# Optimization experiments

Measured on AMD Instinct MI355X. Metric: run time of the kernel, lower is better.

## Reference

```python
import jax, jax.numpy as jnp
import numpy as np

B, S, F = 128, 256, 40
H, D, NH, L, FF = 64, 128, 4, 2, 2048
REG, BIN, NW = 8, 1, 3
NEG = -1e9


def _ln(x, s, b, eps=1e-5):
    m = x.mean(-1, keepdims=True)
    v = ((x - m) ** 2).mean(-1, keepdims=True)
    return (x - m) / jnp.sqrt(v + eps) * s + b


def setup_inputs() -> dict:
    key = jax.random.key(0)
    ks = list(jax.random.split(key, 40))
    k = iter(ks)
    def rn(shape, s=0.05):
        return jax.random.normal(next(k), shape, jnp.float32) * s
    inp = {}
    inp['x'] = jax.random.normal(next(k), (B, S, F), jnp.float32)
    inp['mask'] = jnp.ones((B, S, F), jnp.float32)
    inp['delta'] = jax.random.uniform(next(k), (B, S, F), jnp.float32)
    # GRU params (torch layout: [3H, in], gates order r,z,n)
    inp['gru_w_ih'] = rn((3 * H, 3 * F))
    inp['gru_w_hh'] = rn((3 * H, H))
    inp['gru_b_ih'] = rn((3 * H,))
    inp['gru_b_hh'] = rn((3 * H,))
    inp['dm_w'] = rn((D, H)); inp['dm_b'] = rn((D,))
    # transformer layers stacked on leading dim L
    inp['in_proj_w'] = rn((L, 3 * D, D)); inp['in_proj_b'] = rn((L, 3 * D))
    inp['out_proj_w'] = rn((L, D, D)); inp['out_proj_b'] = rn((L, D))
    inp['lin1_w'] = rn((L, FF, D)); inp['lin1_b'] = rn((L, FF))
    inp['lin2_w'] = rn((L, D, FF)); inp['lin2_b'] = rn((L, D))
    inp['ln1_s'] = jnp.ones((L, D), jnp.float32); inp['ln1_b'] = jnp.zeros((L, D), jnp.float32)
    inp['ln2_s'] = jnp.ones((L, D), jnp.float32); inp['ln2_b'] = jnp.zeros((L, D), jnp.float32)
    inp['score_w'] = rn((1, D)); inp['score_b'] = rn((1,))
    inp['reg_w'] = rn((NW, REG, D)); inp['reg_b'] = rn((NW, REG))
    inp['bin_w'] = rn((NW, BIN, D)); inp['bin_b'] = rn((NW, BIN))
    inp['window_id'] = jax.random.randint(next(k), (B,), 0, NW, jnp.int32)
    return inp


def reference(x, mask, delta, gru_w_ih, gru_w_hh, gru_b_ih, gru_b_hh, dm_w, dm_b,
              in_proj_w, in_proj_b, out_proj_w, out_proj_b, lin1_w, lin1_b,
              lin2_w, lin2_b, ln1_s, ln1_b, ln2_s, ln2_b, score_w, score_b,
              reg_w, reg_b, bin_w, bin_b, window_id):
    inp = jnp.concatenate([x, mask, delta], -1)          # [B,S,3F]
    xw = inp @ gru_w_ih.T + gru_b_ih                      # [B,S,3H] precomputed input gates

    def step(h, xw_t):
        gh = h @ gru_w_hh.T + gru_b_hh
        xr, xz, xn = jnp.split(xw_t, 3, -1)
        hr, hz, hn = jnp.split(gh, 3, -1)
        r = jax.nn.sigmoid(xr + hr)
        zg = jax.nn.sigmoid(xz + hz)
        n = jnp.tanh(xn + r * hn)
        h_new = (1.0 - zg) * n + zg * h
        return h_new, h_new

    h0 = jnp.zeros((x.shape[0], H), x.dtype)
    _, hs = jax.lax.scan(step, h0, jnp.swapaxes(xw, 0, 1))  # [S,B,H]
    z = jnp.swapaxes(hs, 0, 1) @ dm_w.T + dm_b              # [B,S,D]

    time_mask = mask.sum(-1) > 0                            # [B,S] bool
    bias = jnp.where(time_mask[:, None, None, :], 0.0, NEG).astype(z.dtype)
    dh = D // NH
    scale = 1.0 / np.sqrt(dh)

    for l in range(L):  # post-LN torch TransformerEncoderLayer
        qkv = z @ in_proj_w[l].T + in_proj_b[l]
        q, k, v = jnp.split(qkv, 3, -1)
        q = q.reshape(B, S, NH, dh).transpose(0, 2, 1, 3)
        k = k.reshape(B, S, NH, dh).transpose(0, 2, 1, 3)
        v = v.reshape(B, S, NH, dh).transpose(0, 2, 1, 3)
        attn = jax.nn.softmax(jnp.einsum('bhqd,bhkd->bhqk', q, k) * scale + bias, -1)
        o = jnp.einsum('bhqk,bhkd->bhqd', attn, v).transpose(0, 2, 1, 3).reshape(B, S, D)
        z = _ln(z + (o @ out_proj_w[l].T + out_proj_b[l]), ln1_s[l], ln1_b[l])
        ff = jax.nn.relu(z @ lin1_w[l].T + lin1_b[l]) @ lin2_w[l].T + lin2_b[l]
        z = _ln(z + ff, ln2_s[l], ln2_b[l])

    scores = (z @ score_w.T + score_b)[..., 0]              # [B,S]
    scores = jnp.where(time_mask, scores, NEG)
    alpha = jax.nn.softmax(scores, 1)
    pooled = jnp.einsum('bsd,bs->bd', z, alpha)             # [B,D]

    # routed heads: gather 1-of-3 head weights per sample, batched matvec
    y_reg = jnp.einsum('bod,bd->bo', reg_w[window_id], pooled) + reg_b[window_id]
    y_bin = jnp.einsum('bod,bd->bo', bin_w[window_id], pooled) + bin_b[window_id]
    return (y_reg, y_bin)
```

## Files before the change

### kernel.cpp

```cpp
#include <hip/hip_runtime.h>

typedef __attribute__((ext_vector_type(8))) short short8;
typedef __attribute__((ext_vector_type(4))) float f32x4;
typedef unsigned short u16;

#define BB   128
#define SS   256
#define FIN  40
#define HH   64
#define DD   128
#define NHH  4
#define LL   2
#define NEGV (-1e9f)

__device__ __forceinline__ u16 f2b(float f) {
    unsigned u = __float_as_uint(f);
    return (u16)((u + 0x7FFFu + ((u >> 16) & 1u)) >> 16);
}
__device__ __forceinline__ float b2f(u16 u) {
    return __uint_as_float(((unsigned)u) << 16);
}

__global__ __launch_bounds__(256) void cvt_all_kernel(const float* __restrict__ dm_w,
                                                      const float* __restrict__ ip_w,
                                                      const float* __restrict__ op_w,
                                                      const float* __restrict__ l1_w,
                                                      const float* __restrict__ l2_w,
                                                      u16* __restrict__ o_dm, u16* __restrict__ o_ip,
                                                      u16* __restrict__ o_op, u16* __restrict__ o_l1,
                                                      u16* __restrict__ o_l2) {
    int blk = blockIdx.x;
    const float* s; u16* d; int off;
    if      (blk < 4)   { s = dm_w; d = o_dm; off = blk; }
    else if (blk < 52)  { s = ip_w; d = o_ip; off = blk - 4; }
    else if (blk < 68)  { s = op_w; d = o_op; off = blk - 52; }
    else if (blk < 324) { s = l1_w; d = o_l1; off = blk - 68; }
    else                { s = l2_w; d = o_l2; off = blk - 324; }
    int i = (off * 256 + threadIdx.x) * 8;
    float4 a = *(const float4*)&s[i];
    float4 b = *(const float4*)&s[i + 4];
    short8 o;
    o[0] = (short)f2b(a.x); o[1] = (short)f2b(a.y); o[2] = (short)f2b(a.z); o[3] = (short)f2b(a.w);
    o[4] = (short)f2b(b.x); o[5] = (short)f2b(b.y); o[6] = (short)f2b(b.z); o[7] = (short)f2b(b.w);
    *(short8*)&d[i] = o;
}

__global__ __launch_bounds__(256) void tm_kernel(const float* __restrict__ mask,
                                                 float* __restrict__ tm) {
    int i = blockIdx.x * blockDim.x + threadIdx.x;
    if (i >= BB * SS) return;
    const float* m = mask + (size_t)i * FIN;
    float s = 0.f;
    for (int f = 0; f < FIN; ++f) s += m[f];
    tm[i] = (s > 0.f) ? 1.f : 0.f;
}

__global__ __launch_bounds__(192) void xw_kernel(const float* __restrict__ x,
                                                 const float* __restrict__ mask,
                                                 const float* __restrict__ delta,
                                                 const float* __restrict__ w_ih,
                                                 const float* __restrict__ b_ih,
                                                 float* __restrict__ xwt) {
    __shared__ float inp[16][120];
    __shared__ float wl[192][21];
    int group = blockIdx.x >> 8;
    int t = blockIdx.x & 255;
    int tid = threadIdx.x;

    for (int idx = tid; idx < 16 * 120; idx += 192) {
        int r = idx / 120, k = idx % 120;
        size_t g = (size_t)(group * 16 + r) * 256 + t;
        float v;
        if (k < 40)      v = x[g * FIN + k];
        else if (k < 80) v = mask[g * FIN + (k - 40)];
        else             v = delta[g * FIN + (k - 80)];
        inp[r][k] = v;
    }

    float acc[16];
#pragma unroll
    for (int r = 0; r < 16; ++r) acc[r] = 0.f;

    for (int kt = 0; kt < 6; ++kt) {
        __syncthreads();
        for (int idx = tid; idx < 192 * 20; idx += 192) {
            int r = idx / 20, k = idx % 20;
            wl[r][k] = w_ih[(size_t)r * 120 + kt * 20 + k];
        }
        __syncthreads();
#pragma unroll
        for (int kk = 0; kk < 20; ++kk) {
            float w = wl[tid][kk];
            int kg = kt * 20 + kk;
#pragma unroll
            for (int r = 0; r < 16; ++r) acc[r] += w * inp[r][kg];
        }
    }
    float bias = b_ih[tid];
    float* o = xwt + ((size_t)(group * 256 + t) * 192 + tid) * 16;
#pragma unroll
    for (int r = 0; r < 16; r += 4) {
        float4 v = {acc[r] + bias, acc[r + 1] + bias, acc[r + 2] + bias, acc[r + 3] + bias};
        *(float4*)&o[r] = v;
    }
}

__device__ __forceinline__ float gru_gate(float xr, float xz, float xn,
                                          float ar, float az, float an, float hold) {
    float r  = 1.f / (1.f + __expf(-(xr + ar)));
    float zg = 1.f / (1.f + __expf(-(xz + az)));
    float nx = xn + r * an;
    float n  = 2.f / (1.f + __expf(-2.f * nx)) - 1.f;
    return (1.f - zg) * n + zg * hold;
}

__global__ __launch_bounds__(512, 1) void gru_scan_kernel(const float* __restrict__ w_hh,
                                                          const float* __restrict__ b_hh,
                                                          const float* __restrict__ xwt,
                                                          u16* __restrict__ hsb) {
    __shared__ __align__(16) u16 hb[2][16 * 64];
    int b0 = blockIdx.x * 16;
    int tid = threadIdx.x;
    int w = tid >> 6, lane = tid & 63;
    int fr = lane & 15, hi = lane >> 4;
    int cw = w & 3;
    int jg = w >> 2;

    for (int idx = tid; idx < 1024; idx += 512) hb[0][idx] = 0;

    int c = cw * 16 + fr;
    float br_ = b_hh[c], bz_ = b_hh[64 + c], bn_ = b_hh[128 + c];

    short8 wfr[2], wfz[2], wfn[2];
#pragma unroll
    for (int ks = 0; ks < 2; ++ks) {
        int slot = ks * 4 + hi;
        const float* p0 = w_hh + (size_t)c * 64 + slot * 8;
        const float* p1 = w_hh + (size_t)(64 + c) * 64 + slot * 8;
        const float* p2 = w_hh + (size_t)(128 + c) * 64 + slot * 8;
#pragma unroll
        for (int q = 0; q < 8; ++q) {
            wfr[ks][q] = (short)f2b(p0[q]);
            wfz[ks][q] = (short)f2b(p1[q]);
            wfn[ks][q] = (short)f2b(p2[q]);
        }
    }

    const float* xg = xwt + (size_t)blockIdx.x * (256 * 192 * 16);
    int lo = hi * 4 + jg * 2;

    float hrA = 0.f, hrB = 0.f;

    int woA = (lo + 0) * 64 + ((((c >> 3) ^ ((lo + 0) & 7))) << 3) + (c & 7);
    int woB = (lo + 1) * 64 + ((((c >> 3) ^ ((lo + 1) & 7))) << 3) + (c & 7);
    size_t hoA = ((size_t)(b0 + lo + 0) * SS) * 64 + c;
    size_t hoB = ((size_t)(b0 + lo + 1) * SS) * 64 + c;

    float2 axr = *(const float2*)&xg[((size_t)0 * 192 + c) * 16 + lo];
    float2 axz = *(const float2*)&xg[((size_t)0 * 192 + 64 + c) * 16 + lo];
    float2 axn = *(const float2*)&xg[((size_t)0 * 192 + 128 + c) * 16 + lo];
    float2 bxr = *(const float2*)&xg[((size_t)1 * 192 + c) * 16 + lo];
    float2 bxz = *(const float2*)&xg[((size_t)1 * 192 + 64 + c) * 16 + lo];
    float2 bxn = *(const float2*)&xg[((size_t)1 * 192 + 128 + c) * 16 + lo];
    __syncthreads();

    int cur = 0;
    auto step = [&](float2 xr2, float2 xz2, float2 xn2, int t) {
        f32x4 ar = {br_, br_, br_, br_};
        f32x4 az = {bz_, bz_, bz_, bz_};
        f32x4 an = {bn_, bn_, bn_, bn_};
#pragma unroll
        for (int ks = 0; ks < 2; ++ks) {
            int soff = (((ks << 2) + hi) ^ (fr & 7)) << 3;
            short8 af = *(const short8*)&hb[cur][fr * 64 + soff];
            ar = __builtin_amdgcn_mfma_f32_16x16x32_bf16(af, wfr[ks], ar, 0, 0, 0);
            az = __builtin_amdgcn_mfma_f32_16x16x32_bf16(af, wfz[ks], az, 0, 0, 0);
            an = __builtin_amdgcn_mfma_f32_16x16x32_bf16(af, wfn[ks], an, 0, 0, 0);
        }
        float aR0, aR1, aZ0, aZ1, aN0, aN1;
        if (jg == 0) { aR0 = ar[0]; aR1 = ar[1]; aZ0 = az[0]; aZ1 = az[1]; aN0 = an[0]; aN1 = an[1]; }
        else         { aR0 = ar[2]; aR1 = ar[3]; aZ0 = az[2]; aZ1 = az[3]; aN0 = an[2]; aN1 = an[3]; }
        hrA = gru_gate(xr2.x, xz2.x, xn2.x, aR0, aZ0, aN0, hrA);
        hrB = gru_gate(xr2.y, xz2.y, xn2.y, aR1, aZ1, aN1, hrB);
        u16 v0 = f2b(hrA), v1 = f2b(hrB);
        int nxt = cur ^ 1;
        hb[nxt][woA] = v0; hb[nxt][woB] = v1;
        hsb[hoA + (size_t)t * 64] = v0;
        hsb[hoB + (size_t)t * 64] = v1;
        asm volatile("s_waitcnt lgkmcnt(0)\n\ts_barrier" ::: "memory");
        cur = nxt;
    };

    for (int t = 0; t < SS; t += 2) {
        {
            int tp = (t + 2 < SS) ? t + 2 : t;
            float2 nr = *(const float2*)&xg[((size_t)tp * 192 + c) * 16 + lo];
            float2 nz = *(const float2*)&xg[((size_t)tp * 192 + 64 + c) * 16 + lo];
            float2 nn = *(const float2*)&xg[((size_t)tp * 192 + 128 + c) * 16 + lo];
            step(axr, axz, axn, t);
            axr = nr; axz = nz; axn = nn;
        }
        {
            int tp = (t + 3 < SS) ? t + 3 : t + 1;
            float2 nr = *(const float2*)&xg[((size_t)tp * 192 + c) * 16 + lo];
            float2 nz = *(const float2*)&xg[((size_t)tp * 192 + 64 + c) * 16 + lo];
            float2 nn = *(const float2*)&xg[((size_t)tp * 192 + 128 + c) * 16 + lo];
            step(bxr, bxz, bxn, t + 1);
            bxr = nr; bxz = nz; bxn = nn;
        }
    }
}

__device__ __forceinline__ void gl_lds16(const void* g, void* s) {
    __builtin_amdgcn_global_load_lds(
        (const __attribute__((address_space(1))) void*)g,
        (__attribute__((address_space(3))) void*)s, 16, 0, 0);
}

template <int MODE, bool RELU>
__global__ __launch_bounds__(256, 2) void mfma_gemm(const u16* __restrict__ A,
                                                    const u16* __restrict__ W,
                                                    const float* __restrict__ bias,
                                                    float* __restrict__ C,
                                                    u16* __restrict__ Cb,
                                                    const float* __restrict__ lns,
                                                    const float* __restrict__ lnb,
                                                    int M, int N, int K) {
    __shared__ __align__(16) u16 Al[128 * 64];
    __shared__ __align__(16) u16 Bl[128 * 64];
    __shared__ float lred[2][2][128];
    int bm = blockIdx.x, bn = blockIdx.y;
    int tid = threadIdx.x;
    int w = tid >> 6, lane = tid & 63;
    int wrow = (w >> 1) * 64, wcol = (w & 1) * 64;
    int fr = lane & 15, hi = lane >> 4;
    int rl = lane >> 3;
    int sl = lane & 7;
    int ssl = sl ^ rl;

    const u16* Ag = A + ((size_t)bm * 128) * K + ssl * 8;
    const u16* Wg = W + ((size_t)bn * 128) * K + ssl * 8;

    f32x4 acc[4][4];
#pragma unroll
    for (int i = 0; i < 4; ++i)
#pragma unroll
        for (int jj = 0; jj < 4; ++jj) acc[i][jj] = (f32x4){0.f, 0.f, 0.f, 0.f};

    int ar[4], br[4];
#pragma unroll
    for (int m = 0; m < 4; ++m) {
        ar[m] = (wrow + m * 16 + fr) * 64;
        br[m] = (wcol + m * 16 + fr) * 64;
    }
    int swz = (fr & 7);

    for (int kt = 0; kt < K; kt += 64) {
        __syncthreads();
#pragma unroll
        for (int i = 0; i < 4; ++i) {
            int c = w * 4 + i;
            int row = c * 8 + rl;
            gl_lds16(Ag + (size_t)row * K + kt, &Al[c * 512]);
            gl_lds16(Wg + (size_t)row * K + kt, &Bl[c * 512]);
        }
        __syncthreads();
#pragma unroll
        for (int kk = 0; kk < 2; ++kk) {
            short8 a[4], bq[4];
            int soff = (((kk << 2) + hi) ^ swz) << 3;
#pragma unroll
            for (int m = 0; m < 4; ++m)
                a[m] = *(const short8*)&Al[ar[m] + soff];
#pragma unroll
            for (int n = 0; n < 4; ++n)
                bq[n] = *(const short8*)&Bl[br[n] + soff];
#pragma unroll
            for (int m = 0; m < 4; ++m)
#pragma unroll
                for (int n = 0; n < 4; ++n)
                    acc[m][n] = __builtin_amdgcn_mfma_f32_16x16x32_bf16(a[m], bq[n], acc[m][n], 0, 0, 0);
        }
    }

    float bv[4];
#pragma unroll
    for (int n = 0; n < 4; ++n) bv[n] = bias[bn * 128 + wcol + n * 16 + fr];

    if (MODE == 4) {
        float v[4][4][4];
#pragma unroll
        for (int m = 0; m < 4; ++m)
#pragma unroll
            for (int j = 0; j < 4; ++j) {
                int row = bm * 128 + wrow + m * 16 + hi * 4 + j;
#pragma unroll
                for (int n = 0; n < 4; ++n)
                    v[m][n][j] = acc[m][n][j] + bv[n] + C[(size_t)row * 128 + wcol + n * 16 + fr];
            }
#pragma unroll
        for (int m = 0; m < 4; ++m)
#pragma unroll
            for (int j = 0; j < 4; ++j) {
                float s = v[m][0][j] + v[m][1][j] + v[m][2][j] + v[m][3][j];
                float q = v[m][0][j]*v[m][0][j] + v[m][1][j]*v[m][1][j]
                        + v[m][2][j]*v[m][2][j] + v[m][3][j]*v[m][3][j];
#pragma unroll
                for (int off = 1; off <= 8; off <<= 1) {
                    s += __shfl_xor(s, off);
                    q += __shfl_xor(q, off);
                }
                if (fr == 0) {
                    int lrow = wrow + m * 16 + hi * 4 + j;
                    lred[0][w & 1][lrow] = s;
                    lred[1][w & 1][lrow] = q;
                }
            }
        __syncthreads();
        float sv[4], bb[4];
#pragma unroll
        for (int n = 0; n < 4; ++n) {
            sv[n] = lns[wcol + n * 16 + fr];
            bb[n] = lnb[wcol + n * 16 + fr];
        }
#pragma unroll
        for (int m = 0; m < 4; ++m)
#pragma unroll
            for (int j = 0; j < 4; ++j) {
                int lrow = wrow + m * 16 + hi * 4 + j;
                float mean = (lred[0][0][lrow] + lred[0][1][lrow]) * (1.f / 128.f);
                float msq  = (lred[1][0][lrow] + lred[1][1][lrow]) * (1.f / 128.f);
                float rstd = rsqrtf(msq - mean * mean + 1e-5f);
                int row = bm * 128 + lrow;
#pragma unroll
                for (int n = 0; n < 4; ++n) {
                    int col = wcol + n * 16 + fr;
                    float o = (v[m][n][j] - mean) * rstd * sv[n] + bb[n];
                    C[(size_t)row * 128 + col] = o;
                    Cb[(size_t)row * 128 + col] = f2b(o);
                }
            }
    } else {
#pragma unroll
        for (int m = 0; m < 4; ++m) {
#pragma unroll
            for (int j = 0; j < 4; ++j) {
                int row = bm * 128 + wrow + m * 16 + hi * 4 + j;
#pragma unroll
                for (int n = 0; n < 4; ++n) {
                    int col = bn * 128 + wcol + n * 16 + fr;
                    float vv = acc[m][n][j] + bv[n];
                    if (RELU) vv = fmaxf(vv, 0.f);
                    if (MODE & 1) C[(size_t)row * N + col] = vv;
                    if (MODE & 2) Cb[(size_t)row * N + col] = f2b(vv);
                }
            }
        }
    }
}

__global__ __launch_bounds__(256, 1) void ff_fused_kernel(const u16* __restrict__ zbin,
                                                          const u16* __restrict__ w1,
                                                          const float* __restrict__ b1,
                                                          const u16* __restrict__ w2,
                                                          const float* __restrict__ b2,
                                                          const float* __restrict__ lns,
                                                          const float* __restrict__ lnb,
                                                          float* __restrict__ z,
                                                          u16* __restrict__ zbout) {
    __shared__ __align__(16) u16 ZB[2][128 * 64];
    __shared__ __align__(16) u16 W1C[2][128 * 64];
    __shared__ __align__(16) u16 W2C[2][128 * 64];
    __shared__ __align__(16) u16 A1[2][128 * 64];
    __shared__ float lred[2][2][128];
    int bm = blockIdx.x;
    int tid = threadIdx.x;
    int w = tid >> 6, lane = tid & 63;
    int wrow = (w >> 1) * 64, wcol = (w & 1) * 64;
    int fr = lane & 15, hi = lane >> 4;
    int rl = lane >> 3, ssl = (lane & 7) ^ rl;
    int swz = fr & 7;
    int xh = wrow >> 6;

#pragma unroll
    for (int hk = 0; hk < 2; ++hk)
#pragma unroll
        for (int i = 0; i < 4; ++i) {
            int ch = w * 4 + i, row = ch * 8 + rl;
            gl_lds16(zbin + ((size_t)(bm * 128 + row)) * 128 + hk * 64 + ssl * 8, &ZB[hk][ch * 512]);
        }

    f32x4 acc2[4][4];
#pragma unroll
    for (int m = 0; m < 4; ++m)
#pragma unroll
        for (int n = 0; n < 4; ++n) acc2[m][n] = (f32x4){0.f, 0.f, 0.f, 0.f};

    for (int ci = 0; ci < 16; ++ci) {
#pragma unroll
        for (int hk = 0; hk < 2; ++hk)
#pragma unroll
            for (int i = 0; i < 4; ++i) {
                int ch = w * 4 + i, row = ch * 8 + rl;
                gl_lds16(w1 + ((size_t)(ci * 128 + row)) * 128 + hk * 64 + ssl * 8, &W1C[hk][ch * 512]);
                gl_lds16(w2 + ((size_t)row) * 2048 + ci * 128 + hk * 64 + ssl * 8, &W2C[hk][ch * 512]);
            }
        __syncthreads();

        f32x4 acc1[4][4];
#pragma unroll
        for (int m = 0; m < 4; ++m)
#pragma unroll
            for (int n = 0; n < 4; ++n) acc1[m][n] = (f32x4){0.f, 0.f, 0.f, 0.f};
#pragma unroll
        for (int ks = 0; ks < 4; ++ks) {
            int hk = ks >> 1;
            int soff = ((((ks & 1) << 2) + hi) ^ swz) << 3;
            short8 a[4], b[4];
#pragma unroll
            for (int m = 0; m < 4; ++m)
                a[m] = *(const short8*)&W1C[hk][(wrow + m * 16 + fr) * 64 + soff];
#pragma unroll
            for (int n = 0; n < 4; ++n)
                b[n] = *(const short8*)&ZB[hk][(wcol + n * 16 + fr) * 64 + soff];
#pragma unroll
            for (int m = 0; m < 4; ++m)
#pragma unroll
                for (int n = 0; n < 4; ++n)
                    acc1[m][n] = __builtin_amdgcn_mfma_f32_16x16x32_bf16(a[m], b[n], acc1[m][n], 0, 0, 0);
        }
#pragma unroll
        for (int m = 0; m < 4; ++m) {
            int x0 = wrow + m * 16 + hi * 4;
            float4 bb = *(const float4*)&b1[ci * 128 + x0];
            int slot = (x0 & 63) >> 3;
            int wadd = x0 & 7;
#pragma unroll
            for (int n = 0; n < 4; ++n) {
                int r = wcol + n * 16 + fr;
                float v0 = fmaxf(acc1[m][n][0] + bb.x, 0.f);
                float v1 = fmaxf(acc1[m][n][1] + bb.y, 0.f);
                float v2 = fmaxf(acc1[m][n][2] + bb.z, 0.f);
                float v3 = fmaxf(acc1[m][n][3] + bb.w, 0.f);
                uint2 pk;
                pk.x = (unsigned)f2b(v0) | ((unsigned)f2b(v1) << 16);
                pk.y = (unsigned)f2b(v2) | ((unsigned)f2b(v3) << 16);
                *(uint2*)&A1[xh][r * 64 + ((slot ^ (r & 7)) << 3) + wadd] = pk;
            }
        }
        __syncthreads();

#pragma unroll
        for (int ks = 0; ks < 4; ++ks) {
            int hk = ks >> 1;
            int soff = ((((ks & 1) << 2) + hi) ^ swz) << 3;
            short8 a[4], b[4];
#pragma unroll
            for (int m = 0; m < 4; ++m)
                a[m] = *(const short8*)&W2C[hk][(wrow + m * 16 + fr) * 64 + soff];
#pragma unroll
            for (int n = 0; n < 4; ++n)
                b[n] = *(const short8*)&A1[hk][(wcol + n * 16 + fr) * 64 + soff];
#pragma unroll
            for (int m = 0; m < 4; ++m)
#pragma unroll
                for (int n = 0; n < 4; ++n)
                    acc2[m][n] = __builtin_amdgcn_mfma_f32_16x16x32_bf16(a[m], b[n], acc2[m][n], 0, 0, 0);
        }
        __syncthreads();
    }

    float vv[4][4][4];
#pragma unroll
    for (int m = 0; m < 4; ++m) {
        int x0 = wrow + m * 16 + hi * 4;
        float4 bb = *(const float4*)&b2[x0];
#pragma unroll
        for (int n = 0; n < 4; ++n) {
            int y = wcol + n * 16 + fr;
            float4 zo = *(const float4*)&z[((size_t)(bm * 128 + y)) * 128 + x0];
            vv[m][n][0] = acc2[m][n][0] + bb.x + zo.x;
            vv[m][n][1] = acc2[m][n][1] + bb.y + zo.y;
            vv[m][n][2] = acc2[m][n][2] + bb.z + zo.z;
            vv[m][n][3] = acc2[m][n][3] + bb.w + zo.w;
        }
    }
#pragma unroll
    for (int n = 0; n < 4; ++n) {
        float s = 0.f, q = 0.f;
#pragma unroll
        for (int m = 0; m < 4; ++m)
#pragma unroll
            for (int j = 0; j < 4; ++j) { float v = vv[m][n][j]; s += v; q += v * v; }
        s += __shfl_xor(s, 16); s += __shfl_xor(s, 32);
        q += __shfl_xor(q, 16); q += __shfl_xor(q, 32);
        if (hi == 0) {
            int y = wcol + n * 16 + fr;
            lred[0][xh][y] = s;
            lred[1][xh][y] = q;
        }
    }
    __syncthreads();
#pragma unroll
    for (int n = 0; n < 4; ++n) {
        int y = wcol + n * 16 + fr;
        float mean = (lred[0][0][y] + lred[0][1][y]) * (1.f / 128.f);
        float msq  = (lred[1][0][y] + lred[1][1][y]) * (1.f / 128.f);
        float rstd = rsqrtf(msq - mean * mean + 1e-5f);
#pragma unroll
        for (int m = 0; m < 4; ++m) {
            int x0 = wrow + m * 16 + hi * 4;
            float4 sv = *(const float4*)&lns[x0];
            float4 bv = *(const float4*)&lnb[x0];
            float o0 = (vv[m][n][0] - mean) * rstd * sv.x + bv.x;
            float o1 = (vv[m][n][1] - mean) * rstd * sv.y + bv.y;
            float o2 = (vv[m][n][2] - mean) * rstd * sv.z + bv.z;
            float o3 = (vv[m][n][3] - mean) * rstd * sv.w + bv.w;
            size_t zoff = ((size_t)(bm * 128 + y)) * 128 + x0;
            *(float4*)&z[zoff] = (float4){o0, o1, o2, o3};
            uint2 pk;
            pk.x = (unsigned)f2b(o0) | ((unsigned)f2b(o1) << 16);
            pk.y = (unsigned)f2b(o2) | ((unsigned)f2b(o3) << 16);
            *(uint2*)&zbout[zoff] = pk;
        }
    }
}

__global__ __launch_bounds__(256) void attn_mfma_kernel(const u16* __restrict__ qkv,
                                                        const float* __restrict__ tm,
                                                        u16* __restrict__ attno) {
    __shared__ __align__(16) u16 Kl[256 * 40];
    __shared__ __align__(16) u16 Vt[32 * 264];
    __shared__ __align__(16) u16 Pl[4][64 * 72];
    __shared__ float tmb[256];
    int bh = blockIdx.x;
    int b = bh >> 2, hd = bh & 3;
    int tid = threadIdx.x;
    int w = tid >> 6, lane = tid & 63;
    int fr = lane & 15, hi = lane >> 4;
    const u16* base = qkv + (size_t)b * SS * 384 + hd * 32;

    for (int idx = tid; idx < 1024; idx += 256) {
        int r = idx >> 2, s = idx & 3;
        short8 v = *(const short8*)(base + (size_t)r * 384 + 128 + s * 8);
        *(short8*)&Kl[r * 40 + s * 8] = v;
    }
    for (int idx = tid; idx < 1024; idx += 256) {
        int r = idx >> 2, s = idx & 3;
        short8 v = *(const short8*)(base + (size_t)r * 384 + 256 + s * 8);
#pragma unroll
        for (int q = 0; q < 8; ++q) Vt[(s * 8 + q) * 264 + r] = (u16)v[q];
    }
    tmb[tid] = (tm[b * SS + tid] > 0.f) ? 0.f : NEGV;

    int q0 = w * 64;
    short8 qf[4];
#pragma unroll
    for (int m = 0; m < 4; ++m)
        qf[m] = *(const short8*)(base + (size_t)(q0 + m * 16 + fr) * 384 + hi * 8);
    __syncthreads();

    const float scale = 0.17677669529663687f;
    f32x4 accO[4][2];
#pragma unroll
    for (int m = 0; m < 4; ++m) {
        accO[m][0] = (f32x4){0.f, 0.f, 0.f, 0.f};
        accO[m][1] = (f32x4){0.f, 0.f, 0.f, 0.f};
    }
    float den[4][4];
#pragma unroll
    for (int m = 0; m < 4; ++m)
#pragma unroll
        for (int j = 0; j < 4; ++j) den[m][j] = 0.f;

    u16* pw = &Pl[w][0];

    for (int kt = 0; kt < 4; ++kt) {
        f32x4 accS[4][4];
#pragma unroll
        for (int m = 0; m < 4; ++m)
#pragma unroll
            for (int n = 0; n < 4; ++n) accS[m][n] = (f32x4){0.f, 0.f, 0.f, 0.f};
        short8 kf[4];
#pragma unroll
        for (int n = 0; n < 4; ++n)
            kf[n] = *(const short8*)&Kl[(kt * 64 + n * 16 + fr) * 40 + hi * 8];
#pragma unroll
        for (int m = 0; m < 4; ++m)
#pragma unroll
            for (int n = 0; n < 4; ++n)
                accS[m][n] = __builtin_amdgcn_mfma_f32_16x16x32_bf16(qf[m], kf[n], accS[m][n], 0, 0, 0);

        float bias[4];
#pragma unroll
        for (int n = 0; n < 4; ++n) bias[n] = tmb[kt * 64 + n * 16 + fr];

#pragma unroll
        for (int m = 0; m < 4; ++m) {
            float rs0 = 0.f, rs1 = 0.f, rs2 = 0.f, rs3 = 0.f;
#pragma unroll
            for (int n = 0; n < 4; ++n) {
                float p0 = __expf(accS[m][n][0] * scale + bias[n]);
                float p1 = __expf(accS[m][n][1] * scale + bias[n]);
                float p2 = __expf(accS[m][n][2] * scale + bias[n]);
                float p3 = __expf(accS[m][n][3] * scale + bias[n]);
                rs0 += p0; rs1 += p1; rs2 += p2; rs3 += p3;
                int cb = n * 16 + fr;
                pw[(m * 16 + hi * 4 + 0) * 72 + cb] = f2b(p0);
                pw[(m * 16 + hi * 4 + 1) * 72 + cb] = f2b(p1);
                pw[(m * 16 + hi * 4 + 2) * 72 + cb] = f2b(p2);
                pw[(m * 16 + hi * 4 + 3) * 72 + cb] = f2b(p3);
            }
#pragma unroll
            for (int off = 1; off <= 8; off <<= 1) {
                rs0 += __shfl_xor(rs0, off);
                rs1 += __shfl_xor(rs1, off);
                rs2 += __shfl_xor(rs2, off);
                rs3 += __shfl_xor(rs3, off);
            }
            den[m][0] += rs0; den[m][1] += rs1; den[m][2] += rs2; den[m][3] += rs3;
        }
        asm volatile("s_waitcnt lgkmcnt(0)" ::: "memory");

#pragma unroll
        for (int ks = 0; ks < 2; ++ks) {
            short8 pf[4], vf[2];
#pragma unroll
            for (int m = 0; m < 4; ++m)
                pf[m] = *(const short8*)&pw[(m * 16 + fr) * 72 + ks * 32 + hi * 8];
#pragma unroll
            for (int nd = 0; nd < 2; ++nd)
                vf[nd] = *(const short8*)&Vt[(nd * 16 + fr) * 264 + kt * 64 + ks * 32 + hi * 8];
#pragma unroll
            for (int m = 0; m < 4; ++m)
#pragma unroll
                for (int nd = 0; nd < 2; ++nd)
                    accO[m][nd] = __builtin_amdgcn_mfma_f32_16x16x32_bf16(pf[m], vf[nd], accO[m][nd], 0, 0, 0);
        }
    }

    u16* orow = attno + (size_t)(b * SS + q0) * DD + hd * 32;
#pragma unroll
    for (int m = 0; m < 4; ++m)
#pragma unroll
        for (int j = 0; j < 4; ++j) {
            float inv = 1.f / den[m][j];
            int qr = m * 16 + hi * 4 + j;
            orow[(size_t)qr * DD + fr]      = f2b(accO[m][0][j] * inv);
            orow[(size_t)qr * DD + 16 + fr] = f2b(accO[m][1][j] * inv);
        }
}

__global__ __launch_bounds__(256) void pool_all_kernel(const float* __restrict__ z,
                                                       const float* __restrict__ score_w,
                                                       const float* __restrict__ score_b,
                                                       const float* __restrict__ tm,
                                                       const float* __restrict__ reg_w,
                                                       const float* __restrict__ reg_b,
                                                       const float* __restrict__ bin_w,
                                                       const float* __restrict__ bin_b,
                                                       const int* __restrict__ wid,
                                                       float* __restrict__ out) {
    int b = blockIdx.x;
    int tid = threadIdx.x;
    __shared__ float sw[128];
    __shared__ float al[SS];
    __shared__ float red[8];
    __shared__ float pp[2][128];
    __shared__ float p[128];

    if (tid < 128) sw[tid] = score_w[tid];
    __syncthreads();

    const float* zr = z + ((size_t)b * SS + tid) * DD;
    float acc = 0.f;
#pragma unroll
    for (int j = 0; j < 128; j += 4) {
        float4 a = *(const float4*)&zr[j];
        float4 wv = *(const float4*)&sw[j];
        acc += a.x * wv.x + a.y * wv.y + a.z * wv.z + a.w * wv.w;
    }
    float sc = acc + score_b[0];
    sc = (tm[b * SS + tid] > 0.f) ? sc : NEGV;

    float m = sc;
#pragma unroll
    for (int off = 32; off; off >>= 1) m = fmaxf(m, __shfl_xor(m, off));
    if ((tid & 63) == 0) red[tid >> 6] = m;
    __syncthreads();
    m = fmaxf(fmaxf(red[0], red[1]), fmaxf(red[2], red[3]));
    float e = __expf(sc - m);
    float ssum = e;
#pragma unroll
    for (int off = 32; off; off >>= 1) ssum += __shfl_xor(ssum, off);
    if ((tid & 63) == 0) red[4 + (tid >> 6)] = ssum;
    __syncthreads();
    ssum = red[4] + red[5] + red[6] + red[7];
    al[tid] = e / ssum;
    __syncthreads();

    int d = tid & 127, half = tid >> 7;
    float pa = 0.f;
    for (int t = half; t < SS; t += 2) pa += al[t] * z[((size_t)b * SS + t) * DD + d];
    pp[half][d] = pa;
    __syncthreads();
    if (tid < 128) p[tid] = pp[0][tid] + pp[1][tid];
    __syncthreads();

    if (tid < 9) {
        int wi = wid[b];
        const float* wrow;
        float bias;
        if (tid < 8) { wrow = reg_w + ((size_t)wi * 8 + tid) * 128; bias = reg_b[wi * 8 + tid]; }
        else         { wrow = bin_w + (size_t)wi * 128;             bias = bin_b[wi]; }
        float hacc = bias;
        for (int k = 0; k < 128; ++k) hacc += wrow[k] * p[k];
        if (tid < 8) out[b * 8 + tid] = hacc;
        else         out[1024 + b] = hacc;
    }
}

extern "C" void kernel_launch(void* const* d_in, const int* in_sizes, int n_in,
                              void* d_out, int out_size, void* d_ws, size_t ws_size,
                              hipStream_t stream) {
    const float* x         = (const float*)d_in[0];
    const float* mask      = (const float*)d_in[1];
    const float* delta     = (const float*)d_in[2];
    const float* gru_w_ih  = (const float*)d_in[3];
    const float* gru_w_hh  = (const float*)d_in[4];
    const float* gru_b_ih  = (const float*)d_in[5];
    const float* gru_b_hh  = (const float*)d_in[6];
    const float* dm_w      = (const float*)d_in[7];
    const float* dm_b      = (const float*)d_in[8];
    const float* in_proj_w = (const float*)d_in[9];
    const float* in_proj_b = (const float*)d_in[10];
    const float* out_proj_w= (const float*)d_in[11];
    const float* out_proj_b= (const float*)d_in[12];
    const float* lin1_w    = (const float*)d_in[13];
    const float* lin1_b    = (const float*)d_in[14];
    const float* lin2_w    = (const float*)d_in[15];
    const float* lin2_b    = (const float*)d_in[16];
    const float* ln1_s     = (const float*)d_in[17];
    const float* ln1_bb    = (const float*)d_in[18];
    const float* ln2_s     = (const float*)d_in[19];
    const float* ln2_bb    = (const float*)d_in[20];
    const float* score_w   = (const float*)d_in[21];
    const float* score_b   = (const float*)d_in[22];
    const float* reg_w     = (const float*)d_in[23];
    const float* reg_b     = (const float*)d_in[24];
    const float* bin_w     = (const float*)d_in[25];
    const float* bin_b     = (const float*)d_in[26];
    const int*   window_id = (const int*)d_in[27];
    float* out = (float*)d_out;

    char* w8 = (char*)d_ws;
    float* z      = (float*)(w8 + 0);
    u16*   zb     = (u16*)  (w8 + 16777216);
    u16*   hsb    = (u16*)  (w8 + 25165824);
    u16*   wb_dm  = (u16*)  (w8 + 29360128);
    u16*   wb_ip  = (u16*)  (w8 + 29376512);
    u16*   wb_op  = (u16*)  (w8 + 29573120);
    u16*   wb_l1  = (u16*)  (w8 + 29638656);
    u16*   wb_l2  = (u16*)  (w8 + 30687232);
    float* tm     = (float*)(w8 + 31735808);
    float* xwt    = (float*)(w8 + 32063488);
    u16*   qkvb   = (u16*)  (w8 + 32063488);
    u16*   attnob = (u16*)  (w8 + 57229312);

    cvt_all_kernel<<<580, 256, 0, stream>>>(dm_w, in_proj_w, out_proj_w, lin1_w, lin2_w,
                                            wb_dm, wb_ip, wb_op, wb_l1, wb_l2);

    tm_kernel<<<(BB * SS + 255) / 256, 256, 0, stream>>>(mask, tm);
    xw_kernel<<<2048, 192, 0, stream>>>(x, mask, delta, gru_w_ih, gru_b_ih, xwt);
    gru_scan_kernel<<<8, 512, 0, stream>>>(gru_w_hh, gru_b_hh, xwt, hsb);

    mfma_gemm<3, false><<<dim3(256, 1), 256, 0, stream>>>(
        hsb, wb_dm, dm_b, z, zb, nullptr, nullptr, 32768, 128, 64);

    for (int l = 0; l < LL; ++l) {
        mfma_gemm<2, false><<<dim3(256, 3), 256, 0, stream>>>(
            zb, wb_ip + (size_t)l * 49152, in_proj_b + l * 384, nullptr, qkvb,
            nullptr, nullptr, 32768, 384, 128);
        attn_mfma_kernel<<<BB * NHH, 256, 0, stream>>>(qkvb, tm, attnob);
        mfma_gemm<4, false><<<dim3(256, 1), 256, 0, stream>>>(
            attnob, wb_op + (size_t)l * 16384, out_proj_b + l * 128, z, zb,
            ln1_s + l * 128, ln1_bb + l * 128, 32768, 128, 128);
        ff_fused_kernel<<<256, 256, 0, stream>>>(
            zb, wb_l1 + (size_t)l * 262144, lin1_b + l * 2048,
            wb_l2 + (size_t)l * 262144, lin2_b + l * 128,
            ln2_s + l * 128, ln2_bb + l * 128, z, zb);
    }

    pool_all_kernel<<<BB, 256, 0, stream>>>(z, score_w, score_b, tm,
                                            reg_w, reg_b, bin_w, bin_b, window_id, out);
}
```

Baseline: 544.4 us.

## Stage GRU hidden-state outputs in LDS and flush with vectorized stores

The GRU scan no longer writes each timestep's bf16 hidden values straight to global memory as scattered 2-byte stores. It buffers 8 timesteps in a shared-memory staging area and then writes them out with coalesced 16-byte vector stores. The input-gate prefetch distance also grows from 2 to 4 steps. This cuts the number of small global store instructions on the latency-bound sequential scan, at the cost of 16KB more LDS, an extra barrier every 8 steps, and more registers.

```diff
diff --git a/kernel.cpp b/kernel.cpp
--- a/kernel.cpp
+++ b/kernel.cpp
@@ -119,6 +119,7 @@
                                                           const float* __restrict__ xwt,
                                                           u16* __restrict__ hsb) {
     __shared__ __align__(16) u16 hb[2][16 * 64];
+    __shared__ __align__(16) u16 hstage[8][16 * 64];
     int b0 = blockIdx.x * 16;
     int tid = threadIdx.x;
     int w = tid >> 6, lane = tid & 63;
@@ -153,19 +154,20 @@
 
     int woA = (lo + 0) * 64 + ((((c >> 3) ^ ((lo + 0) & 7))) << 3) + (c & 7);
     int woB = (lo + 1) * 64 + ((((c >> 3) ^ ((lo + 1) & 7))) << 3) + (c & 7);
-    size_t hoA = ((size_t)(b0 + lo + 0) * SS) * 64 + c;
-    size_t hoB = ((size_t)(b0 + lo + 1) * SS) * 64 + c;
-
-    float2 axr = *(const float2*)&xg[((size_t)0 * 192 + c) * 16 + lo];
-    float2 axz = *(const float2*)&xg[((size_t)0 * 192 + 64 + c) * 16 + lo];
-    float2 axn = *(const float2*)&xg[((size_t)0 * 192 + 128 + c) * 16 + lo];
-    float2 bxr = *(const float2*)&xg[((size_t)1 * 192 + c) * 16 + lo];
-    float2 bxz = *(const float2*)&xg[((size_t)1 * 192 + 64 + c) * 16 + lo];
-    float2 bxn = *(const float2*)&xg[((size_t)1 * 192 + 128 + c) * 16 + lo];
+    int soA = (lo + 0) * 64 + c;
+    int soB = (lo + 1) * 64 + c;
+
+    float2 pxr[4], pxz[4], pxn[4];
+#pragma unroll
+    for (int u = 0; u < 4; ++u) {
+        pxr[u] = *(const float2*)&xg[((size_t)u * 192 + c) * 16 + lo];
+        pxz[u] = *(const float2*)&xg[((size_t)u * 192 + 64 + c) * 16 + lo];
+        pxn[u] = *(const float2*)&xg[((size_t)u * 192 + 128 + c) * 16 + lo];
+    }
     __syncthreads();
 
     int cur = 0;
-    auto step = [&](float2 xr2, float2 xz2, float2 xn2, int t) {
+    auto step = [&](float2 xr2, float2 xz2, float2 xn2, int ts) {
         f32x4 ar = {br_, br_, br_, br_};
         f32x4 az = {bz_, bz_, bz_, bz_};
         f32x4 an = {bn_, bn_, bn_, bn_};
@@ -185,29 +187,30 @@
         u16 v0 = f2b(hrA), v1 = f2b(hrB);
         int nxt = cur ^ 1;
         hb[nxt][woA] = v0; hb[nxt][woB] = v1;
-        hsb[hoA + (size_t)t * 64] = v0;
-        hsb[hoB + (size_t)t * 64] = v1;
+        hstage[ts][soA] = v0; hstage[ts][soB] = v1;
         asm volatile("s_waitcnt lgkmcnt(0)\n\ts_barrier" ::: "memory");
         cur = nxt;
     };
 
-    for (int t = 0; t < SS; t += 2) {
-        {
-            int tp = (t + 2 < SS) ? t + 2 : t;
+    for (int t = 0; t < SS; t += 8) {
+#pragma unroll
+        for (int u = 0; u < 8; ++u) {
+            int tp = t + u + 4; tp = (tp < SS) ? tp : (SS - 1);
             float2 nr = *(const float2*)&xg[((size_t)tp * 192 + c) * 16 + lo];
             float2 nz = *(const float2*)&xg[((size_t)tp * 192 + 64 + c) * 16 + lo];
             float2 nn = *(const float2*)&xg[((size_t)tp * 192 + 128 + c) * 16 + lo];
-            step(axr, axz, axn, t);
-            axr = nr; axz = nz; axn = nn;
-        }
-        {
-            int tp = (t + 3 < SS) ? t + 3 : t + 1;
-            float2 nr = *(const float2*)&xg[((size_t)tp * 192 + c) * 16 + lo];
-            float2 nz = *(const float2*)&xg[((size_t)tp * 192 + 64 + c) * 16 + lo];
-            float2 nn = *(const float2*)&xg[((size_t)tp * 192 + 128 + c) * 16 + lo];
-            step(bxr, bxz, bxn, t + 1);
-            bxr = nr; bxz = nz; bxn = nn;
-        }
+            step(pxr[u & 3], pxz[u & 3], pxn[u & 3], u);
+            pxr[u & 3] = nr; pxz[u & 3] = nz; pxn[u & 3] = nn;
+        }
+#pragma unroll
+        for (int f = 0; f < 2; ++f) {
+            int idx = tid + f * 512;
+            int c8 = idx & 7, pair = idx >> 3;
+            int ts = pair >> 4, row = pair & 15;
+            short8 v = *(const short8*)&hstage[ts][row * 64 + c8 * 8];
+            *(short8*)&hsb[((size_t)(b0 + row) * SS + t + ts) * 64 + c8 * 8] = v;
+        }
+        asm volatile("s_waitcnt lgkmcnt(0)\n\ts_barrier" ::: "memory");
     }
 }
 
```

New measurement: 503.0 us. -7.6%, faster.
